# Kernel optimization log

Measured on AMD Instinct MI355X. Metric: run time of the kernel, lower is better.

## Reference

```python
import jax, jax.numpy as jnp
import numpy as np

B, T, V, D, C, O = 64, 128, 32, 128, 10000, 512


def setup_inputs() -> dict:
    key = jax.random.key(0)
    ks = jax.random.split(key, 14)
    s = 1.0 / np.sqrt(D)
    # ragged visit sequences: codes in [1, C), padded visits are all-zero codes
    codes = jax.random.randint(ks[0], (B, T, V), 1, C, dtype=jnp.int32)
    lengths = jax.random.randint(ks[1], (B,), 1, T + 1, dtype=jnp.int32)
    visit_mask = (jnp.arange(T)[None, :] < lengths[:, None])
    codes_x = codes * visit_mask[:, :, None].astype(jnp.int32)
    emb = (jax.random.normal(ks[2], (C, D), jnp.float32) * 0.02).at[0].set(0.0)
    return {
        "codes_x": codes_x,
        "emb": emb,
        "a_kernel": jax.random.normal(ks[3], (D, 3 * D), jnp.float32) * s,
        "a_rec": jax.random.normal(ks[4], (D, 3 * D), jnp.float32) * s,
        "a_bias": jnp.zeros((2, 3 * D), jnp.float32),
        "b_kernel": jax.random.normal(ks[5], (D, 3 * D), jnp.float32) * s,
        "b_rec": jax.random.normal(ks[6], (D, 3 * D), jnp.float32) * s,
        "b_bias": jnp.zeros((2, 3 * D), jnp.float32),
        "alpha_w": jax.random.normal(ks[7], (D, 1), jnp.float32) * s,
        "alpha_b": jnp.zeros((1,), jnp.float32),
        "beta_w": jax.random.normal(ks[8], (D, D), jnp.float32) * s,
        "beta_b": jnp.zeros((D,), jnp.float32),
        "cls_w": jax.random.normal(ks[9], (D, O), jnp.float32) * s,
        "cls_b": jnp.zeros((O,), jnp.float32),
    }


def gru(x, mask, kernel, rec, bias):
    """Keras GRU (reset_after=True), masked: carries state+output through padded steps.
    x: [B,T,D], mask: [B,T] bool -> [B,T,D]."""
    bi, br = bias[0], bias[1]
    xp = x @ kernel + bi  # [B,T,3D] precomputed input projection

    def step(h, inp):
        xp_t, m_t = inp
        hp = h @ rec + br
        xz, xr, xh = jnp.split(xp_t, 3, axis=-1)
        hz, hr, hh = jnp.split(hp, 3, axis=-1)
        z = jax.nn.sigmoid(xz + hz)
        r = jax.nn.sigmoid(xr + hr)
        hcand = jnp.tanh(xh + r * hh)
        h_new = z * h + (1.0 - z) * hcand
        h_out = jnp.where(m_t[:, None], h_new, h)
        return h_out, h_out

    h0 = jnp.zeros((x.shape[0], rec.shape[0]), x.dtype)
    _, ys = jax.lax.scan(step, h0, (jnp.swapaxes(xp, 0, 1), jnp.swapaxes(mask, 0, 1)))
    return jnp.swapaxes(ys, 0, 1)


def retain_forward(codes_x, emb, a_kernel, a_rec, a_bias, b_kernel, b_rec, b_bias,
                   alpha_w, alpha_b, beta_w, beta_b, cls_w, cls_b):
    x = emb[codes_x].sum(axis=2)                     # [B,T,D] visit embeddings
    mask = x.sum(axis=-1) != 0                       # [B,T] visit mask
    lengths = mask.sum(axis=-1)                      # [B]
    # masked reverse: rx[b, j] = x[b, lengths[b]-1-j] for j < lengths[b], else 0
    t = x.shape[1]
    idx = lengths[:, None] - 1 - jnp.arange(t)[None, :]  # [B,T]
    valid = idx >= 0
    rx = jnp.take_along_axis(x, jnp.clip(idx, 0, t - 1)[:, :, None], axis=1)
    rx = rx * valid[:, :, None].astype(x.dtype)
    # dual GRU attention (dropout inactive at inference)
    g = gru(rx, mask, a_kernel, a_rec, a_bias)
    h = gru(rx, mask, b_kernel, b_rec, b_bias)
    attn_alpha = jax.nn.softmax(g @ alpha_w + alpha_b, axis=1)   # [B,T,1]
    attn_beta = jnp.tanh(h @ beta_w + beta_b)                    # [B,T,D]
    c = jnp.sum(attn_alpha * attn_beta * x, axis=1)              # [B,D]
    return c @ cls_w + cls_b                                     # [B,O]


def reference(codes_x, emb, a_kernel, a_rec, a_bias, b_kernel, b_rec, b_bias,
              alpha_w, alpha_b, beta_w, beta_b, cls_w, cls_b):
    return retain_forward(codes_x, emb, a_kernel, a_rec, a_bias, b_kernel, b_rec,
                          b_bias, alpha_w, alpha_b, beta_w, beta_b, cls_w, cls_b)
```

## Files before the change

kernel.cpp:

```cpp
#include <hip/hip_runtime.h>
#include <math.h>

#define BATCH 64
#define TT 128
#define VV 32
#define DD 128
#define OO 512
#define N3 384
#define NN 768

#define OFF_X      0u
#define OFF_XPC    1048576u
#define OFF_GSEQ   7340032u
#define OFF_HSEQ   8388608u
#define OFF_INTS   9437184u
#define OFF_ALPHA  9453632u
#define OFF_CPART  9461824u

__global__ __launch_bounds__(128) void k_gather(const int* __restrict__ codes,
        const float* __restrict__ emb, float* __restrict__ x, int* __restrict__ mask) {
    int bt = blockIdx.x;
    int d = threadIdx.x;
    const int* cp = codes + (size_t)bt * VV;
    float acc = 0.f;
    #pragma unroll 8
    for (int v = 0; v < VV; ++v) {
        int code = cp[v];
        acc += emb[(size_t)code * DD + d];
    }
    x[(size_t)bt * DD + d] = acc;
    float s = acc;
    #pragma unroll
    for (int off = 32; off; off >>= 1) s += __shfl_xor(s, off);
    __shared__ float red[2];
    if ((d & 63) == 0) red[d >> 6] = s;
    __syncthreads();
    if (d == 0) mask[bt] = ((red[0] + red[1]) != 0.0f) ? 1 : 0;
}

__global__ __launch_bounds__(128) void k_len(const int* __restrict__ mask,
        int* __restrict__ lengths, int* __restrict__ ridx) {
    int b = blockIdx.x, t = threadIdx.x;
    int m = mask[b * TT + t];
    unsigned long long bal = __ballot(m != 0);
    __shared__ int cnt[2];
    if ((t & 63) == 0) cnt[t >> 6] = __popcll(bal);
    __syncthreads();
    int len = cnt[0] + cnt[1];
    if (t == 0) lengths[b] = len;
    ridx[b * TT + t] = len - 1 - t;
}

__global__ __launch_bounds__(256) void k_xp(const float* __restrict__ x,
        const float* __restrict__ akern, const float* __restrict__ bkern,
        const float* __restrict__ abias, const float* __restrict__ bbias,
        float* __restrict__ xpc) {
    __shared__ __attribute__((aligned(16))) float As[32][68];
    __shared__ __attribute__((aligned(16))) float Bs[32][68];
    int mb = blockIdx.x, nb = blockIdx.y;
    int n0 = nb * 64;
    int tid = threadIdx.x;
    int tx = tid & 15, ty = tid >> 4;
    float acc[4][4] = {};
    for (int k0 = 0; k0 < DD; k0 += 32) {
        #pragma unroll
        for (int i = 0; i < 2; ++i) {
            int s = tid * 2 + i;
            int row = s >> 3, kk = (s & 7) * 4;
            float4 v = *reinterpret_cast<const float4*>(x + (size_t)(mb * 64 + row) * DD + k0 + kk);
            As[kk][row] = v.x; As[kk+1][row] = v.y; As[kk+2][row] = v.z; As[kk+3][row] = v.w;
        }
        #pragma unroll
        for (int i = 0; i < 2; ++i) {
            int s = tid * 2 + i;
            int kk = s >> 4, c = (s & 15) * 4;
            int n = n0 + c;
            const float* src = (n < N3) ? (akern + (size_t)(k0 + kk) * N3 + n)
                                        : (bkern + (size_t)(k0 + kk) * N3 + (n - N3));
            *reinterpret_cast<float4*>(&Bs[kk][c]) = *reinterpret_cast<const float4*>(src);
        }
        __syncthreads();
        #pragma unroll
        for (int kk = 0; kk < 32; ++kk) {
            float4 a = *reinterpret_cast<const float4*>(&As[kk][ty * 4]);
            float4 bv = *reinterpret_cast<const float4*>(&Bs[kk][tx * 4]);
            float av[4] = {a.x, a.y, a.z, a.w};
            float bw[4] = {bv.x, bv.y, bv.z, bv.w};
            #pragma unroll
            for (int i2 = 0; i2 < 4; ++i2)
                #pragma unroll
                for (int j2 = 0; j2 < 4; ++j2)
                    acc[i2][j2] = fmaf(av[i2], bw[j2], acc[i2][j2]);
        }
        __syncthreads();
    }
    int nbase = n0 + tx * 4;
    float4 bias;
    if (nbase < N3) bias = *reinterpret_cast<const float4*>(abias + nbase);
    else            bias = *reinterpret_cast<const float4*>(bbias + (nbase - N3));
    #pragma unroll
    for (int i2 = 0; i2 < 4; ++i2) {
        int m = mb * 64 + ty * 4 + i2;
        float4 o;
        o.x = acc[i2][0] + bias.x; o.y = acc[i2][1] + bias.y;
        o.z = acc[i2][2] + bias.z; o.w = acc[i2][3] + bias.w;
        *reinterpret_cast<float4*>(xpc + (size_t)m * NN + nbase) = o;
    }
}

__device__ __forceinline__ float fast_sigmoid(float x) {
    return 1.f / (1.f + __expf(-x));
}
__device__ __forceinline__ float fast_tanh(float x) {
    float xc = fminf(fmaxf(x, -15.f), 15.f);
    float e2 = __expf(2.f * xc);
    return (e2 - 1.f) / (e2 + 1.f);
}

#define LOADW(i) \
    float w##i##_x, w##i##_y, w##i##_z, w##i##_w; \
    { const float* rp = rec + (size_t)(k0 + 4 * i) * N3 + j; \
      w##i##_x = rp[0]; w##i##_y = rp[N3]; w##i##_z = rp[2 * N3]; w##i##_w = rp[3 * N3]; } \
    asm volatile("" : "+v"(w##i##_x), "+v"(w##i##_y), "+v"(w##i##_z), "+v"(w##i##_w));
#define DOTW(i) { float4 hv = *reinterpret_cast<const float4*>(&h_lds[k0 + 4 * i]); \
    a0 = fmaf(hv.x, w##i##_x, a0); a1 = fmaf(hv.y, w##i##_y, a1); \
    a2 = fmaf(hv.z, w##i##_z, a2); a3 = fmaf(hv.w, w##i##_w, a3); }

__global__ __launch_bounds__(768) __attribute__((amdgpu_waves_per_eu(3, 3)))
void k_gru(
        const float* __restrict__ arec, const float* __restrict__ abias,
        const float* __restrict__ brec, const float* __restrict__ bbias,
        const float* __restrict__ xpc, const int* __restrict__ mask,
        const int* __restrict__ ridx, float* __restrict__ gseq, float* __restrict__ hseq) {
    int b = blockIdx.x & 63;
    int gru = blockIdx.x >> 6;
    const float* rec  = gru ? brec : arec;
    const float* bias = gru ? bbias : abias;
    float* seq = gru ? hseq : gseq;
    int t = threadIdx.x;
    int half = (t >= N3) ? 1 : 0;
    int j = t - half * N3;
    int k0 = half * 64;
    LOADW(0)  LOADW(1)  LOADW(2)  LOADW(3)
    LOADW(4)  LOADW(5)  LOADW(6)  LOADW(7)
    LOADW(8)  LOADW(9)  LOADW(10) LOADW(11)
    LOADW(12) LOADW(13) LOADW(14) LOADW(15)
    __shared__ __attribute__((aligned(16))) float h_lds[DD];
    __shared__ float part[768];
    __shared__ int smask[TT];
    __shared__ int sridx[TT];
    if (t < TT) { smask[t] = mask[b * TT + t]; sridx[t] = ridx[b * TT + t]; }
    if (t < DD) h_lds[t] = 0.f;
    float bz_r = 0.f, br_r = 0.f, bh_r = 0.f, bz_i = 0.f, br_i = 0.f, bh_i = 0.f;
    if (t < DD) {
        bz_r = bias[N3 + t];  br_r = bias[N3 + DD + t];  bh_r = bias[N3 + 2 * DD + t];
        bz_i = bias[t];       br_i = bias[DD + t];       bh_i = bias[2 * DD + t];
    }
    float hreg = 0.f;
    __syncthreads();
    const float* xpb = xpc + (size_t)b * TT * NN + gru * N3;
    for (int step = 0; step < TT; ++step) {
        int m = smask[step];
        if (!m) {
            if (t < DD) seq[(size_t)(b * TT + step) * DD + t] = hreg;
            continue;
        }
        float xz = 0.f, xr = 0.f, xh = 0.f;
        if (t < DD) {
            int row = sridx[step];
            if (row >= 0) {
                const float* xrow = xpb + (size_t)row * NN;
                xz = xrow[t]; xr = xrow[DD + t]; xh = xrow[2 * DD + t];
            } else {
                xz = bz_i; xr = br_i; xh = bh_i;
            }
        }
        float a0 = 0.f, a1 = 0.f, a2 = 0.f, a3 = 0.f;
        DOTW(0)  DOTW(1)  DOTW(2)  DOTW(3)
        DOTW(4)  DOTW(5)  DOTW(6)  DOTW(7)
        DOTW(8)  DOTW(9)  DOTW(10) DOTW(11)
        DOTW(12) DOTW(13) DOTW(14) DOTW(15)
        part[t] = (a0 + a1) + (a2 + a3);
        __syncthreads();
        if (t < DD) {
            float hz = part[t]           + part[t + N3]          + bz_r;
            float hr = part[t + DD]      + part[t + N3 + DD]     + br_r;
            float hh = part[t + 2 * DD]  + part[t + N3 + 2 * DD] + bh_r;
            float z = fast_sigmoid(xz + hz);
            float r = fast_sigmoid(xr + hr);
            float hc = fast_tanh(xh + r * hh);
            float hnew = z * hreg + (1.f - z) * hc;
            hreg = hnew;
            h_lds[t] = hnew;
            seq[(size_t)(b * TT + step) * DD + t] = hnew;
        }
        __syncthreads();
    }
}

__global__ __launch_bounds__(128) void k_alpha(const float* __restrict__ gseq,
        const float* __restrict__ alpha_w, const float* __restrict__ alpha_b,
        float* __restrict__ alpha) {
    int b = blockIdx.x, t = threadIdx.x;
    __shared__ float aw[DD];
    aw[t] = alpha_w[t];
    __syncthreads();
    const float* g = gseq + (size_t)(b * TT + t) * DD;
    float acc = 0.f;
    #pragma unroll
    for (int k = 0; k < DD; k += 4) {
        float4 gv = *reinterpret_cast<const float4*>(g + k);
        acc = fmaf(gv.x, aw[k],     acc);
        acc = fmaf(gv.y, aw[k + 1], acc);
        acc = fmaf(gv.z, aw[k + 2], acc);
        acc = fmaf(gv.w, aw[k + 3], acc);
    }
    float logit = acc + alpha_b[0];
    float mx = logit;
    #pragma unroll
    for (int off = 32; off; off >>= 1) mx = fmaxf(mx, __shfl_xor(mx, off));
    __shared__ float redm[2];
    if ((t & 63) == 0) redm[t >> 6] = mx;
    __syncthreads();
    mx = fmaxf(redm[0], redm[1]);
    float e = expf(logit - mx);
    float s = e;
    #pragma unroll
    for (int off = 32; off; off >>= 1) s += __shfl_xor(s, off);
    __shared__ float reds[2];
    if ((t & 63) == 0) reds[t >> 6] = s;
    __syncthreads();
    alpha[b * TT + t] = e / (reds[0] + reds[1]);
}

__global__ __launch_bounds__(128) void k_beta(const float* __restrict__ hseq,
        const float* __restrict__ x, const float* __restrict__ beta_w,
        const float* __restrict__ beta_b, const float* __restrict__ alpha,
        float* __restrict__ cpart) {
    __shared__ __attribute__((aligned(16))) float bw[DD][DD];
    __shared__ __attribute__((aligned(16))) float hr[4][DD];
    __shared__ float cred[4][DD];
    int b = blockIdx.x >> 3, grp = blockIdx.x & 7;
    int tid = threadIdx.x;
    for (int i = tid; i < DD * DD / 4; i += 128) {
        float4 v = *reinterpret_cast<const float4*>(beta_w + (size_t)i * 4);
        *reinterpret_cast<float4*>(&bw[0][0] + (size_t)i * 4) = v;
    }
    int trow = tid >> 5, dq = (tid & 31) * 4;
    float bb0 = beta_b[dq], bb1 = beta_b[dq + 1], bb2 = beta_b[dq + 2], bb3 = beta_b[dq + 3];
    float c0 = 0.f, c1 = 0.f, c2 = 0.f, c3 = 0.f;
    for (int tg = 0; tg < 4; ++tg) {
        int t = grp * 16 + tg * 4 + trow;
        size_t rowoff = (size_t)(b * TT + t) * DD;
        float4 hv = *reinterpret_cast<const float4*>(hseq + rowoff + dq);
        __syncthreads();
        *reinterpret_cast<float4*>(&hr[trow][dq]) = hv;
        __syncthreads();
        float a0 = 0.f, a1 = 0.f, a2 = 0.f, a3 = 0.f;
        #pragma unroll 8
        for (int k = 0; k < DD; ++k) {
            float hk = hr[trow][k];
            float4 w = *reinterpret_cast<const float4*>(&bw[k][dq]);
            a0 = fmaf(hk, w.x, a0); a1 = fmaf(hk, w.y, a1);
            a2 = fmaf(hk, w.z, a2); a3 = fmaf(hk, w.w, a3);
        }
        float al = alpha[b * TT + t];
        float4 xv = *reinterpret_cast<const float4*>(x + rowoff + dq);
        c0 = fmaf(al * tanhf(a0 + bb0), xv.x, c0);
        c1 = fmaf(al * tanhf(a1 + bb1), xv.y, c1);
        c2 = fmaf(al * tanhf(a2 + bb2), xv.z, c2);
        c3 = fmaf(al * tanhf(a3 + bb3), xv.w, c3);
    }
    cred[trow][dq] = c0; cred[trow][dq + 1] = c1;
    cred[trow][dq + 2] = c2; cred[trow][dq + 3] = c3;
    __syncthreads();
    if (tid < 32) {
        #pragma unroll
        for (int i = 0; i < 4; ++i) {
            int d = tid * 4 + i;
            float sum = cred[0][d] + cred[1][d] + cred[2][d] + cred[3][d];
            cpart[(size_t)(b * 8 + grp) * DD + d] = sum;
        }
    }
}

__global__ __launch_bounds__(256) void k_out(const float* __restrict__ cpart,
        const float* __restrict__ cls_w, const float* __restrict__ cls_b,
        float* __restrict__ out) {
    __shared__ float cl[DD];
    int b = blockIdx.x, tid = threadIdx.x;
    if (tid < DD) {
        float s = 0.f;
        #pragma unroll
        for (int p = 0; p < 8; ++p) s += cpart[(size_t)(b * 8 + p) * DD + tid];
        cl[tid] = s;
    }
    __syncthreads();
    #pragma unroll
    for (int rep = 0; rep < 2; ++rep) {
        int o = tid + rep * 256;
        float acc = cls_b[o];
        #pragma unroll 8
        for (int k = 0; k < DD; ++k)
            acc = fmaf(cl[k], cls_w[(size_t)k * OO + o], acc);
        out[(size_t)b * OO + o] = acc;
    }
}

extern "C" void kernel_launch(void* const* d_in, const int* in_sizes, int n_in,
                              void* d_out, int out_size, void* d_ws, size_t ws_size,
                              hipStream_t stream) {
    const int*   codes   = (const int*)d_in[0];
    const float* emb     = (const float*)d_in[1];
    const float* akern   = (const float*)d_in[2];
    const float* arec    = (const float*)d_in[3];
    const float* abias   = (const float*)d_in[4];
    const float* bkern   = (const float*)d_in[5];
    const float* brec    = (const float*)d_in[6];
    const float* bbias   = (const float*)d_in[7];
    const float* alpha_w = (const float*)d_in[8];
    const float* alpha_b = (const float*)d_in[9];
    const float* beta_w  = (const float*)d_in[10];
    const float* beta_b  = (const float*)d_in[11];
    const float* cls_w   = (const float*)d_in[12];
    const float* cls_b   = (const float*)d_in[13];
    float* ws   = (float*)d_ws;
    float* x    = ws + OFF_X;
    float* xpc  = ws + OFF_XPC;
    float* gseq = ws + OFF_GSEQ;
    float* hseq = ws + OFF_HSEQ;
    int*   ints = (int*)(ws + OFF_INTS);
    int* mask    = ints;
    int* ridx    = ints + 8192;
    int* lengths = ints + 16384;
    float* alpha = ws + OFF_ALPHA;
    float* cpart = ws + OFF_CPART;
    float* out   = (float*)d_out;

    k_gather<<<BATCH * TT, 128, 0, stream>>>(codes, emb, x, mask);
    k_len<<<BATCH, 128, 0, stream>>>(mask, lengths, ridx);
    dim3 g3(128, 12);
    k_xp<<<g3, 256, 0, stream>>>(x, akern, bkern, abias, bbias, xpc);
    k_gru<<<128, 768, 0, stream>>>(arec, abias, brec, bbias, xpc, mask, ridx, gseq, hseq);
    k_alpha<<<BATCH, 128, 0, stream>>>(gseq, alpha_w, alpha_b, alpha);
    k_beta<<<BATCH * 8, 128, 0, stream>>>(hseq, x, beta_w, beta_b, alpha, cpart);
    k_out<<<BATCH, 256, 0, stream>>>(cpart, cls_w, cls_b, out);
}
```

Before: 187.8 us.

## Process two batch rows per GRU block to reuse register-resident recurrent weights

Each GRU block now runs the recurrence for a pair of batch rows. It reuses the same register-held recurrent weight slice for two hidden-state vectors, with a separate accumulator set per row, and halves the grid from 128 to 64 blocks. The goal is to cut duplicated weight loads and the number of resident blocks. The cost is doubled FMA and LDS reads per step on the serial critical path. The loop also now runs to the longer of the two sequences, and occupancy drops on a GPU that already had idle CUs.

```diff
diff --git a/kernel.cpp b/kernel.cpp
--- a/kernel.cpp
+++ b/kernel.cpp
@@ -122,18 +122,23 @@
     { const float* rp = rec + (size_t)(k0 + 4 * i) * N3 + j; \
       w##i##_x = rp[0]; w##i##_y = rp[N3]; w##i##_z = rp[2 * N3]; w##i##_w = rp[3 * N3]; } \
     asm volatile("" : "+v"(w##i##_x), "+v"(w##i##_y), "+v"(w##i##_z), "+v"(w##i##_w));
-#define DOTW(i) { float4 hv = *reinterpret_cast<const float4*>(&h_lds[k0 + 4 * i]); \
-    a0 = fmaf(hv.x, w##i##_x, a0); a1 = fmaf(hv.y, w##i##_y, a1); \
-    a2 = fmaf(hv.z, w##i##_z, a2); a3 = fmaf(hv.w, w##i##_w, a3); }
-
-__global__ __launch_bounds__(768) __attribute__((amdgpu_waves_per_eu(3, 3)))
+#define DOTW2(i) { \
+    float4 hv0 = *reinterpret_cast<const float4*>(&h_lds2[0][k0 + 4 * i]); \
+    float4 hv1 = *reinterpret_cast<const float4*>(&h_lds2[1][k0 + 4 * i]); \
+    a0 = fmaf(hv0.x, w##i##_x, a0); a1 = fmaf(hv0.y, w##i##_y, a1); \
+    a2 = fmaf(hv0.z, w##i##_z, a2); a3 = fmaf(hv0.w, w##i##_w, a3); \
+    e0 = fmaf(hv1.x, w##i##_x, e0); e1 = fmaf(hv1.y, w##i##_y, e1); \
+    e2 = fmaf(hv1.z, w##i##_z, e2); e3 = fmaf(hv1.w, w##i##_w, e3); }
+
+__global__ __launch_bounds__(768, 3)
 void k_gru(
         const float* __restrict__ arec, const float* __restrict__ abias,
         const float* __restrict__ brec, const float* __restrict__ bbias,
         const float* __restrict__ xpc, const int* __restrict__ mask,
         const int* __restrict__ ridx, float* __restrict__ gseq, float* __restrict__ hseq) {
-    int b = blockIdx.x & 63;
-    int gru = blockIdx.x >> 6;
+    int pair = blockIdx.x & 31;
+    int gru = blockIdx.x >> 5;
+    int b0 = pair * 2, b1 = pair * 2 + 1;
     const float* rec  = gru ? brec : arec;
     const float* bias = gru ? bbias : abias;
     float* seq = gru ? hseq : gseq;
@@ -145,54 +150,70 @@
     LOADW(4)  LOADW(5)  LOADW(6)  LOADW(7)
     LOADW(8)  LOADW(9)  LOADW(10) LOADW(11)
     LOADW(12) LOADW(13) LOADW(14) LOADW(15)
-    __shared__ __attribute__((aligned(16))) float h_lds[DD];
-    __shared__ float part[768];
-    __shared__ int smask[TT];
-    __shared__ int sridx[TT];
-    if (t < TT) { smask[t] = mask[b * TT + t]; sridx[t] = ridx[b * TT + t]; }
-    if (t < DD) h_lds[t] = 0.f;
-    float bz_r = 0.f, br_r = 0.f, bh_r = 0.f, bz_i = 0.f, br_i = 0.f, bh_i = 0.f;
-    if (t < DD) {
-        bz_r = bias[N3 + t];  br_r = bias[N3 + DD + t];  bh_r = bias[N3 + 2 * DD + t];
-        bz_i = bias[t];       br_i = bias[DD + t];       bh_i = bias[2 * DD + t];
+    __shared__ __attribute__((aligned(16))) float h_lds2[2][DD];
+    __shared__ float part2[2][768];
+    __shared__ int smask2[2][TT];
+    __shared__ int sridx2[2][TT];
+    if (t < TT)          { smask2[0][t] = mask[b0 * TT + t]; sridx2[0][t] = ridx[b0 * TT + t]; }
+    else if (t < 2 * TT) { int u = t - TT;
+                           smask2[1][u] = mask[b1 * TT + u]; sridx2[1][u] = ridx[b1 * TT + u]; }
+    if (t < 2 * DD) h_lds2[t >> 7][t & 127] = 0.f;
+    float bz_r = 0.f, br_r = 0.f, bh_r = 0.f;
+    if (t < 2 * DD) {
+        int d = t & 127;
+        bz_r = bias[N3 + d];  br_r = bias[N3 + DD + d];  bh_r = bias[N3 + 2 * DD + d];
     }
     float hreg = 0.f;
     __syncthreads();
-    const float* xpb = xpc + (size_t)b * TT * NN + gru * N3;
+    const float* xpb0 = xpc + (size_t)b0 * TT * NN + gru * N3;
+    const float* xpb1 = xpc + (size_t)b1 * TT * NN + gru * N3;
     for (int step = 0; step < TT; ++step) {
-        int m = smask[step];
-        if (!m) {
-            if (t < DD) seq[(size_t)(b * TT + step) * DD + t] = hreg;
+        int m0 = smask2[0][step], m1 = smask2[1][step];
+        if (!(m0 | m1)) {
+            if (t < 2 * DD) {
+                int bi = t >> 7, d = t & 127;
+                seq[(size_t)((bi ? b1 : b0) * TT + step) * DD + d] = hreg;
+            }
             continue;
         }
         float xz = 0.f, xr = 0.f, xh = 0.f;
-        if (t < DD) {
-            int row = sridx[step];
-            if (row >= 0) {
-                const float* xrow = xpb + (size_t)row * NN;
-                xz = xrow[t]; xr = xrow[DD + t]; xh = xrow[2 * DD + t];
+        if (t < 2 * DD) {
+            int bi = t >> 7, d = t & 127;
+            int mi = bi ? m1 : m0;
+            if (mi) {
+                int row = sridx2[bi][step];
+                const float* xrow = (bi ? xpb1 : xpb0) + (size_t)row * NN;
+                xz = xrow[d]; xr = xrow[DD + d]; xh = xrow[2 * DD + d];
+            }
+        }
+        float a0 = 0.f, a1 = 0.f, a2 = 0.f, a3 = 0.f;
+        float e0 = 0.f, e1 = 0.f, e2 = 0.f, e3 = 0.f;
+        DOTW2(0)  DOTW2(1)  DOTW2(2)  DOTW2(3)
+        DOTW2(4)  DOTW2(5)  DOTW2(6)  DOTW2(7)
+        DOTW2(8)  DOTW2(9)  DOTW2(10) DOTW2(11)
+        DOTW2(12) DOTW2(13) DOTW2(14) DOTW2(15)
+        part2[0][t] = (a0 + a1) + (a2 + a3);
+        part2[1][t] = (e0 + e1) + (e2 + e3);
+        __syncthreads();
+        if (t < 2 * DD) {
+            int bi = t >> 7, d = t & 127;
+            int mi = bi ? m1 : m0;
+            size_t so = (size_t)((bi ? b1 : b0) * TT + step) * DD + d;
+            if (mi) {
+                const float* pp = &part2[bi][0];
+                float hz = pp[d]          + pp[d + N3]          + bz_r;
+                float hr = pp[d + DD]     + pp[d + N3 + DD]     + br_r;
+                float hh = pp[d + 2 * DD] + pp[d + N3 + 2 * DD] + bh_r;
+                float z = fast_sigmoid(xz + hz);
+                float r = fast_sigmoid(xr + hr);
+                float hc = fast_tanh(xh + r * hh);
+                float hnew = z * hreg + (1.f - z) * hc;
+                hreg = hnew;
+                h_lds2[bi][d] = hnew;
+                seq[so] = hnew;
             } else {
-                xz = bz_i; xr = br_i; xh = bh_i;
+                seq[so] = hreg;
             }
-        }
-        float a0 = 0.f, a1 = 0.f, a2 = 0.f, a3 = 0.f;
-        DOTW(0)  DOTW(1)  DOTW(2)  DOTW(3)
-        DOTW(4)  DOTW(5)  DOTW(6)  DOTW(7)
-        DOTW(8)  DOTW(9)  DOTW(10) DOTW(11)
-        DOTW(12) DOTW(13) DOTW(14) DOTW(15)
-        part[t] = (a0 + a1) + (a2 + a3);
-        __syncthreads();
-        if (t < DD) {
-            float hz = part[t]           + part[t + N3]          + bz_r;
-            float hr = part[t + DD]      + part[t + N3 + DD]     + br_r;
-            float hh = part[t + 2 * DD]  + part[t + N3 + 2 * DD] + bh_r;
-            float z = fast_sigmoid(xz + hz);
-            float r = fast_sigmoid(xr + hr);
-            float hc = fast_tanh(xh + r * hh);
-            float hnew = z * hreg + (1.f - z) * hc;
-            hreg = hnew;
-            h_lds[t] = hnew;
-            seq[(size_t)(b * TT + step) * DD + t] = hnew;
         }
         __syncthreads();
     }
@@ -341,7 +362,7 @@
     k_len<<<BATCH, 128, 0, stream>>>(mask, lengths, ridx);
     dim3 g3(128, 12);
     k_xp<<<g3, 256, 0, stream>>>(x, akern, bkern, abias, bbias, xpc);
-    k_gru<<<128, 768, 0, stream>>>(arec, abias, brec, bbias, xpc, mask, ridx, gseq, hseq);
+    k_gru<<<64, 768, 0, stream>>>(arec, abias, brec, bbias, xpc, mask, ridx, gseq, hseq);
     k_alpha<<<BATCH, 128, 0, stream>>>(gseq, alpha_w, alpha_b, alpha);
     k_beta<<<BATCH * 8, 128, 0, stream>>>(hseq, x, beta_w, beta_b, alpha, cpart);
     k_out<<<BATCH, 256, 0, stream>>>(cpart, cls_w, cls_b, out);
```

Result: slower. 219.6 us (+16.9%).
